# Performance work log

Measured on AMD Instinct MI355X. Metric: run time of the kernel, lower is better.

## Reference

```python
import jax, jax.numpy as jnp
import numpy as np

CLAMP_MIN = 1e-12
CLAMP_MAX = 1e12


def setup_inputs() -> dict:
    key = jax.random.key(0)
    k1, k2, k3 = jax.random.split(key, 3)
    N, C, H, W = 32, 11, 384, 384
    x = jax.random.normal(k1, (N, C, H, W), dtype=jnp.float32)
    centers = jax.random.normal(k2, (N, C, H, W), dtype=jnp.float32)
    labels = jax.random.randint(k3, (N, H, W), 0, C, dtype=jnp.int64)
    return {"x": x, "centers": centers, "labels": labels}


def reference(x, centers, labels):
    # x, centers: (N, C, H, W); labels: (N, H, W) int
    N, C, H, W = x.shape
    # res[n,c] = x[n,c]^2 + centers[n,c]^2 - 2 * x[n,c] @ centers[n,c]
    # (single batched matmul replaces the original per-(i,j) addmm loop)
    res = x * x + centers * centers - 2.0 * jnp.matmul(x, centers)
    # softmax over class dim, then max over class dim -> (N, H, W)
    res_max = jnp.max(jax.nn.softmax(res, axis=1), axis=1)
    dist = res_max * labels.astype(res_max.dtype)
    loss = jnp.sum(jnp.clip(dist, CLAMP_MIN, CLAMP_MAX)) / (H * W * N)
    return loss
```

## Files before the change

kernel.cpp:

```cpp
#include <hip/hip_runtime.h>
#include <stdint.h>

typedef __attribute__((ext_vector_type(8))) short short8;
typedef __attribute__((ext_vector_type(4))) float floatx4;
typedef __attribute__((ext_vector_type(4))) unsigned short u16x4;

#define Hh 384
#define Ww 384
#define Cc 11
#define Nn 32
#define PITCH 72

__device__ __forceinline__ unsigned short f2bf(float f) {
  union { float f; uint32_t u; } z; z.f = f;
  return (unsigned short)(z.u >> 16);
}
__device__ __forceinline__ float bf2f(unsigned short b) {
  union { uint32_t u; float f; } z; z.u = ((uint32_t)b) << 16;
  return z.f;
}

__global__ __launch_bounds__(256, 4)
void center_loss(const float* __restrict__ X, const float* __restrict__ Cen,
                 const int* __restrict__ Lab, float* __restrict__ Out) {
  __shared__ __align__(16) unsigned short Alds[64 * PITCH];
  __shared__ __align__(16) unsigned short Blds[64 * PITCH];
  __shared__ float red[4];

  const int bx   = blockIdx.x;
  const int xcd  = bx & 7;
  const int slot = bx >> 3;
  const int grp  = slot / 36;
  const int t36  = slot - grp * 36;
  const int n    = xcd + (grp << 3);
  const int ib = t36 / 6;
  const int jb = t36 - ib * 6;
  const int i0 = ib << 6, j0 = jb << 6;

  const int t   = threadIdx.x;
  const int l   = t & 63;
  const int w   = t >> 6;
  const int wr  = (w >> 1) << 5;
  const int wc  = (w & 1) << 5;
  const int q4  = l >> 4;
  const int l16 = l & 15;
  const int sa  = t & 15;
  const int sr  = t >> 4;

  const size_t plane = (size_t)Hh * Ww;
  const float* xbase = X   + (size_t)n * Cc * plane;
  const float* cbase = Cen + (size_t)n * Cc * plane;

  float m[16], s[16];
#pragma unroll
  for (int i = 0; i < 16; ++i) { m[i] = -3.0e38f; s[i] = 0.0f; }

  floatx4 acc[2][2];
  float ev[16];
#pragma unroll
  for (int a = 0; a < 2; ++a)
#pragma unroll
    for (int b = 0; b < 2; ++b) acc[a][b] = (floatx4){0.f, 0.f, 0.f, 0.f};
#pragma unroll
  for (int i = 0; i < 16; ++i) ev[i] = 0.0f;

  float4 pa[4];
  float  pb[16];

  {
    const float* ap = xbase + (size_t)(i0 + sr) * Ww + (sa << 2);
#pragma unroll
    for (int p = 0; p < 4; ++p)
      pa[p] = *reinterpret_cast<const float4*>(ap + (size_t)(p * 16) * Ww);
#pragma unroll
    for (int p = 0; p < 2; ++p) {
      const int kbase = (w << 3) + (p << 5);
      const float* bp = cbase + (size_t)kbase * Ww + j0 + l;
#pragma unroll
      for (int u = 0; u < 8; ++u) pb[p * 8 + u] = bp[(size_t)u * Ww];
    }
  }

  int c = 0, kb = 0;
  for (int it = 0; it < 66; ++it) {
    __syncthreads();

#pragma unroll
    for (int p = 0; p < 4; ++p) {
      u16x4 pk;
      pk.x = f2bf(pa[p].x); pk.y = f2bf(pa[p].y);
      pk.z = f2bf(pa[p].z); pk.w = f2bf(pa[p].w);
      *reinterpret_cast<u16x4*>(&Alds[(sr + 16 * p) * PITCH + (sa << 2)]) = pk;
    }
#pragma unroll
    for (int p = 0; p < 2; ++p) {
      const int kbase = (w << 3) + (p << 5);
      short8 pk;
#pragma unroll
      for (int u = 0; u < 8; ++u) pk[u] = (short)f2bf(pb[p * 8 + u]);
      *reinterpret_cast<short8*>(&Blds[l * PITCH + kbase]) = pk;
    }

    int kn = kb + 1, cn = c;
    if (kn == 6) { kn = 0; cn = c + 1; }
    float4 na[4];
    float  nb[16];
    if (it < 65) {
      const float* xb = xbase + (size_t)cn * plane;
      const float* cb = cbase + (size_t)cn * plane;
      const float* ap = xb + (size_t)(i0 + sr) * Ww + (kn << 6) + (sa << 2);
#pragma unroll
      for (int p = 0; p < 4; ++p)
        na[p] = *reinterpret_cast<const float4*>(ap + (size_t)(p * 16) * Ww);
#pragma unroll
      for (int p = 0; p < 2; ++p) {
        const int kbase = (w << 3) + (p << 5);
        const float* bp = cb + (size_t)((kn << 6) + kbase) * Ww + j0 + l;
#pragma unroll
        for (int u = 0; u < 8; ++u) nb[p * 8 + u] = bp[(size_t)u * Ww];
      }
    }

    __syncthreads();

    if (kb == jb) {
#pragma unroll
      for (int fr = 0; fr < 2; ++fr)
#pragma unroll
        for (int fc = 0; fc < 2; ++fc)
#pragma unroll
          for (int r = 0; r < 4; ++r) {
            const int idx = ((fr << 1) + fc) * 4 + r;
            const int pr = wr + (fr << 4) + (q4 << 2) + r;
            const int pc = wc + (fc << 4) + l16;
            float xv = bf2f(Alds[pr * PITCH + pc]);
            ev[idx] += xv * xv;
          }
    }
    if (kb == ib) {
#pragma unroll
      for (int fr = 0; fr < 2; ++fr)
#pragma unroll
        for (int fc = 0; fc < 2; ++fc)
#pragma unroll
          for (int r = 0; r < 4; ++r) {
            const int idx = ((fr << 1) + fc) * 4 + r;
            const int pr = wr + (fr << 4) + (q4 << 2) + r;
            const int pc = wc + (fc << 4) + l16;
            float cv = bf2f(Blds[pc * PITCH + pr]);
            ev[idx] += cv * cv;
          }
    }

#pragma unroll
    for (int ks = 0; ks < 2; ++ks) {
      const int ko = (ks << 5) + (q4 << 3);
      short8 a0 = *reinterpret_cast<const short8*>(&Alds[(wr +      l16) * PITCH + ko]);
      short8 a1 = *reinterpret_cast<const short8*>(&Alds[(wr + 16 + l16) * PITCH + ko]);
      short8 b0 = *reinterpret_cast<const short8*>(&Blds[(wc +      l16) * PITCH + ko]);
      short8 b1 = *reinterpret_cast<const short8*>(&Blds[(wc + 16 + l16) * PITCH + ko]);
      acc[0][0] = __builtin_amdgcn_mfma_f32_16x16x32_bf16(a0, b0, acc[0][0], 0, 0, 0);
      acc[0][1] = __builtin_amdgcn_mfma_f32_16x16x32_bf16(a0, b1, acc[0][1], 0, 0, 0);
      acc[1][0] = __builtin_amdgcn_mfma_f32_16x16x32_bf16(a1, b0, acc[1][0], 0, 0, 0);
      acc[1][1] = __builtin_amdgcn_mfma_f32_16x16x32_bf16(a1, b1, acc[1][1], 0, 0, 0);
    }

    if (kb == 5) {
#pragma unroll
      for (int fr = 0; fr < 2; ++fr)
#pragma unroll
        for (int fc = 0; fc < 2; ++fc)
#pragma unroll
          for (int r = 0; r < 4; ++r) {
            const int idx = ((fr << 1) + fc) * 4 + r;
            float res = ev[idx] - 2.0f * acc[fr][fc][r];
            float mi = m[idx];
            if (res <= mi) {
              s[idx] += __expf(res - mi);
            } else {
              s[idx] = s[idx] * __expf(mi - res) + 1.0f;
              m[idx] = res;
            }
            acc[fr][fc][r] = 0.0f;
            ev[idx] = 0.0f;
          }
    }

    kb = kn; c = cn;
#pragma unroll
    for (int p = 0; p < 4; ++p) pa[p] = na[p];
#pragma unroll
    for (int p = 0; p < 16; ++p) pb[p] = nb[p];
  }

  float local = 0.0f;
  const int* lb = Lab + (size_t)n * plane;
#pragma unroll
  for (int fr = 0; fr < 2; ++fr)
#pragma unroll
    for (int fc = 0; fc < 2; ++fc)
#pragma unroll
      for (int r = 0; r < 4; ++r) {
        const int idx = ((fr << 1) + fc) * 4 + r;
        const int pr = i0 + wr + (fr << 4) + (q4 << 2) + r;
        const int pc = j0 + wc + (fc << 4) + l16;
        float val = 1.0f / s[idx];
        float d = val * (float)lb[pr * Ww + pc];
        d = fminf(fmaxf(d, 1e-12f), 1e12f);
        local += d;
      }
#pragma unroll
  for (int off = 32; off > 0; off >>= 1) local += __shfl_down(local, off, 64);
  if (l == 0) red[w] = local;
  __syncthreads();
  if (t == 0) {
    float bs = (red[0] + red[1] + red[2] + red[3]) * (1.0f / 4718592.0f);
    atomicAdd(Out, bs);
  }
}

extern "C" void kernel_launch(void* const* d_in, const int* in_sizes, int n_in,
                              void* d_out, int out_size, void* d_ws, size_t ws_size,
                              hipStream_t stream) {
  const float* X   = (const float*)d_in[0];
  const float* Cen = (const float*)d_in[1];
  const int*   Lab = (const int*)d_in[2];
  float* Out = (float*)d_out;
  hipMemsetAsync(Out, 0, (size_t)out_size * sizeof(float), stream);
  hipLaunchKernelGGL(center_loss, dim3(Nn * 36), dim3(256), 0, stream,
                     X, Cen, Lab, Out);
}
```

Measured before the change: 495.7 us.

## Double-buffer LDS tiles with single barrier and fold norms into accumulator

Switches the A/B staging tiles to two LDS buffers so staging of the next tile overlaps compute of the current one, needing one custom barrier per tile that waits only on LDS counters. The squared-norm terms are subtracted directly into the MFMA accumulators instead of kept in separate registers. C-tile global loads become float2 per thread with a new thread mapping. LDS usage doubles, which may limit how many blocks fit per CU.

```diff
diff --git a/kernel.cpp b/kernel.cpp
--- a/kernel.cpp
+++ b/kernel.cpp
@@ -20,11 +20,17 @@
   return z.f;
 }
 
+#define BAR() do {                                          \
+    asm volatile("s_waitcnt lgkmcnt(0)" ::: "memory");      \
+    __builtin_amdgcn_s_barrier();                           \
+    asm volatile("" ::: "memory");                          \
+  } while (0)
+
 __global__ __launch_bounds__(256, 4)
 void center_loss(const float* __restrict__ X, const float* __restrict__ Cen,
                  const int* __restrict__ Lab, float* __restrict__ Out) {
-  __shared__ __align__(16) unsigned short Alds[64 * PITCH];
-  __shared__ __align__(16) unsigned short Blds[64 * PITCH];
+  __shared__ __align__(16) unsigned short Alds[2][64 * PITCH];
+  __shared__ __align__(16) unsigned short Blds[2][64 * PITCH];
   __shared__ float red[4];
 
   const int bx   = blockIdx.x;
@@ -44,154 +50,133 @@
   const int wc  = (w & 1) << 5;
   const int q4  = l >> 4;
   const int l16 = l & 15;
+  const int sr  = t >> 4;
   const int sa  = t & 15;
-  const int sr  = t >> 4;
+  const int jp  = t & 31;
+  const int kc  = t >> 5;
 
   const size_t plane = (size_t)Hh * Ww;
-  const float* xbase = X   + (size_t)n * Cc * plane;
-  const float* cbase = Cen + (size_t)n * Cc * plane;
+  const float* xrow = X   + (size_t)n * Cc * plane + (size_t)(i0 + sr) * Ww + (sa << 2);
+  const float* crow = Cen + (size_t)n * Cc * plane + (size_t)(kc << 3) * Ww + j0 + (jp << 1);
 
   float m[16], s[16];
 #pragma unroll
   for (int i = 0; i < 16; ++i) { m[i] = -3.0e38f; s[i] = 0.0f; }
 
   floatx4 acc[2][2];
-  float ev[16];
 #pragma unroll
   for (int a = 0; a < 2; ++a)
 #pragma unroll
     for (int b = 0; b < 2; ++b) acc[a][b] = (floatx4){0.f, 0.f, 0.f, 0.f};
-#pragma unroll
-  for (int i = 0; i < 16; ++i) ev[i] = 0.0f;
 
   float4 pa[4];
-  float  pb[16];
-
-  {
-    const float* ap = xbase + (size_t)(i0 + sr) * Ww + (sa << 2);
-#pragma unroll
-    for (int p = 0; p < 4; ++p)
-      pa[p] = *reinterpret_cast<const float4*>(ap + (size_t)(p * 16) * Ww);
-#pragma unroll
-    for (int p = 0; p < 2; ++p) {
-      const int kbase = (w << 3) + (p << 5);
-      const float* bp = cbase + (size_t)kbase * Ww + j0 + l;
-#pragma unroll
-      for (int u = 0; u < 8; ++u) pb[p * 8 + u] = bp[(size_t)u * Ww];
-    }
+  float2 pb[8];
+
+#define LOADT(CC, KK) do {                                                     \
+    const float* ap_ = xrow + (size_t)(CC) * plane + ((KK) << 6);              \
+    pa[0] = *reinterpret_cast<const float4*>(ap_);                             \
+    pa[1] = *reinterpret_cast<const float4*>(ap_ + 16 * Ww);                   \
+    pa[2] = *reinterpret_cast<const float4*>(ap_ + 32 * Ww);                   \
+    pa[3] = *reinterpret_cast<const float4*>(ap_ + 48 * Ww);                   \
+    const float* bp_ = crow + (size_t)(CC) * plane + (size_t)((KK) << 6) * Ww; \
+    _Pragma("unroll")                                                          \
+    for (int u_ = 0; u_ < 8; ++u_)                                             \
+      pb[u_] = *reinterpret_cast<const float2*>(bp_ + (size_t)u_ * Ww);        \
+  } while (0)
+
+#define STAGE(WB) do {                                                         \
+    _Pragma("unroll")                                                          \
+    for (int p_ = 0; p_ < 4; ++p_) {                                           \
+      u16x4 pk_;                                                               \
+      pk_.x = f2bf(pa[p_].x); pk_.y = f2bf(pa[p_].y);                          \
+      pk_.z = f2bf(pa[p_].z); pk_.w = f2bf(pa[p_].w);                          \
+      *reinterpret_cast<u16x4*>(&Alds[WB][(sr + 16 * p_) * PITCH + (sa << 2)]) = pk_; \
+    }                                                                          \
+    short8 s0_, s1_;                                                           \
+    _Pragma("unroll")                                                          \
+    for (int u_ = 0; u_ < 8; ++u_) {                                           \
+      s0_[u_] = (short)f2bf(pb[u_].x);                                         \
+      s1_[u_] = (short)f2bf(pb[u_].y);                                         \
+    }                                                                          \
+    *reinterpret_cast<short8*>(&Blds[WB][(jp << 1) * PITCH + (kc << 3)]) = s0_;       \
+    *reinterpret_cast<short8*>(&Blds[WB][((jp << 1) + 1) * PITCH + (kc << 3)]) = s1_; \
+  } while (0)
+
+#define COMPUTE(RB) do {                                                       \
+    if (kb == jb) {                       \
+      _Pragma("unroll") for (int fr_ = 0; fr_ < 2; ++fr_)                      \
+      _Pragma("unroll") for (int fc_ = 0; fc_ < 2; ++fc_)                      \
+      _Pragma("unroll") for (int r_ = 0; r_ < 4; ++r_) {                       \
+        const int pr_ = wr + (fr_ << 4) + (q4 << 2) + r_;                      \
+        const int pc_ = wc + (fc_ << 4) + l16;                                 \
+        float xv_ = bf2f(Alds[RB][pr_ * PITCH + pc_]);                         \
+        acc[fr_][fc_][r_] -= 0.5f * xv_ * xv_;                                 \
+      }                                                                        \
+    }                                                                          \
+    if (kb == ib) {         \
+      _Pragma("unroll") for (int fr_ = 0; fr_ < 2; ++fr_)                      \
+      _Pragma("unroll") for (int fc_ = 0; fc_ < 2; ++fc_)                      \
+      _Pragma("unroll") for (int r_ = 0; r_ < 4; ++r_) {                       \
+        const int pr_ = wr + (fr_ << 4) + (q4 << 2) + r_;                      \
+        const int pc_ = wc + (fc_ << 4) + l16;                                 \
+        float cv_ = bf2f(Blds[RB][pc_ * PITCH + pr_]);                         \
+        acc[fr_][fc_][r_] -= 0.5f * cv_ * cv_;                                 \
+      }                                                                        \
+    }                                                                          \
+    _Pragma("unroll") for (int ks_ = 0; ks_ < 2; ++ks_) {                      \
+      const int ko_ = (ks_ << 5) + (q4 << 3);                                  \
+      short8 a0_ = *reinterpret_cast<const short8*>(&Alds[RB][(wr +      l16) * PITCH + ko_]); \
+      short8 a1_ = *reinterpret_cast<const short8*>(&Alds[RB][(wr + 16 + l16) * PITCH + ko_]); \
+      short8 b0_ = *reinterpret_cast<const short8*>(&Blds[RB][(wc +      l16) * PITCH + ko_]); \
+      short8 b1_ = *reinterpret_cast<const short8*>(&Blds[RB][(wc + 16 + l16) * PITCH + ko_]); \
+      acc[0][0] = __builtin_amdgcn_mfma_f32_16x16x32_bf16(a0_, b0_, acc[0][0], 0, 0, 0); \
+      acc[0][1] = __builtin_amdgcn_mfma_f32_16x16x32_bf16(a0_, b1_, acc[0][1], 0, 0, 0); \
+      acc[1][0] = __builtin_amdgcn_mfma_f32_16x16x32_bf16(a1_, b0_, acc[1][0], 0, 0, 0); \
+      acc[1][1] = __builtin_amdgcn_mfma_f32_16x16x32_bf16(a1_, b1_, acc[1][1], 0, 0, 0); \
+    }                                                                          \
+    if (kb == 5) {                \
+      _Pragma("unroll") for (int fr_ = 0; fr_ < 2; ++fr_)                      \
+      _Pragma("unroll") for (int fc_ = 0; fc_ < 2; ++fc_)                      \
+      _Pragma("unroll") for (int r_ = 0; r_ < 4; ++r_) {                       \
+        const int idx_ = ((fr_ << 1) + fc_) * 4 + r_;                          \
+        float res_ = -2.0f * acc[fr_][fc_][r_];                                \
+        float mi_ = m[idx_];                                                   \
+        if (res_ <= mi_) {                                                     \
+          s[idx_] += __expf(res_ - mi_);                                       \
+        } else {                                                               \
+          s[idx_] = s[idx_] * __expf(mi_ - res_) + 1.0f;                       \
+          m[idx_] = res_;                                                      \
+        }                                                                      \
+        acc[fr_][fc_][r_] = 0.0f;                                              \
+      }                                                                        \
+    }                                                                          \
+    ++kb; if (kb == 6) kb = 0;                                                 \
+  } while (0)
+
+  LOADT(0, 0);
+  STAGE(0);
+  LOADT(0, 1);
+  BAR();
+
+  int kb = 0;
+  int kbL = 2, cL = 0;
+
+  for (int mi = 0; mi < 32; ++mi) {
+    STAGE(1);
+    LOADT(cL, kbL);
+    ++kbL; if (kbL == 6) { kbL = 0; ++cL; }
+    COMPUTE(0);
+    BAR();
+    STAGE(0);
+    LOADT(cL, kbL);
+    ++kbL; if (kbL == 6) { kbL = 0; ++cL; }
+    COMPUTE(1);
+    BAR();
   }
-
-  int c = 0, kb = 0;
-  for (int it = 0; it < 66; ++it) {
-    __syncthreads();
-
-#pragma unroll
-    for (int p = 0; p < 4; ++p) {
-      u16x4 pk;
-      pk.x = f2bf(pa[p].x); pk.y = f2bf(pa[p].y);
-      pk.z = f2bf(pa[p].z); pk.w = f2bf(pa[p].w);
-      *reinterpret_cast<u16x4*>(&Alds[(sr + 16 * p) * PITCH + (sa << 2)]) = pk;
-    }
-#pragma unroll
-    for (int p = 0; p < 2; ++p) {
-      const int kbase = (w << 3) + (p << 5);
-      short8 pk;
-#pragma unroll
-      for (int u = 0; u < 8; ++u) pk[u] = (short)f2bf(pb[p * 8 + u]);
-      *reinterpret_cast<short8*>(&Blds[l * PITCH + kbase]) = pk;
-    }
-
-    int kn = kb + 1, cn = c;
-    if (kn == 6) { kn = 0; cn = c + 1; }
-    float4 na[4];
-    float  nb[16];
-    if (it < 65) {
-      const float* xb = xbase + (size_t)cn * plane;
-      const float* cb = cbase + (size_t)cn * plane;
-      const float* ap = xb + (size_t)(i0 + sr) * Ww + (kn << 6) + (sa << 2);
-#pragma unroll
-      for (int p = 0; p < 4; ++p)
-        na[p] = *reinterpret_cast<const float4*>(ap + (size_t)(p * 16) * Ww);
-#pragma unroll
-      for (int p = 0; p < 2; ++p) {
-        const int kbase = (w << 3) + (p << 5);
-        const float* bp = cb + (size_t)((kn << 6) + kbase) * Ww + j0 + l;
-#pragma unroll
-        for (int u = 0; u < 8; ++u) nb[p * 8 + u] = bp[(size_t)u * Ww];
-      }
-    }
-
-    __syncthreads();
-
-    if (kb == jb) {
-#pragma unroll
-      for (int fr = 0; fr < 2; ++fr)
-#pragma unroll
-        for (int fc = 0; fc < 2; ++fc)
-#pragma unroll
-          for (int r = 0; r < 4; ++r) {
-            const int idx = ((fr << 1) + fc) * 4 + r;
-            const int pr = wr + (fr << 4) + (q4 << 2) + r;
-            const int pc = wc + (fc << 4) + l16;
-            float xv = bf2f(Alds[pr * PITCH + pc]);
-            ev[idx] += xv * xv;
-          }
-    }
-    if (kb == ib) {
-#pragma unroll
-      for (int fr = 0; fr < 2; ++fr)
-#pragma unroll
-        for (int fc = 0; fc < 2; ++fc)
-#pragma unroll
-          for (int r = 0; r < 4; ++r) {
-            const int idx = ((fr << 1) + fc) * 4 + r;
-            const int pr = wr + (fr << 4) + (q4 << 2) + r;
-            const int pc = wc + (fc << 4) + l16;
-            float cv = bf2f(Blds[pc * PITCH + pr]);
-            ev[idx] += cv * cv;
-          }
-    }
-
-#pragma unroll
-    for (int ks = 0; ks < 2; ++ks) {
-      const int ko = (ks << 5) + (q4 << 3);
-      short8 a0 = *reinterpret_cast<const short8*>(&Alds[(wr +      l16) * PITCH + ko]);
-      short8 a1 = *reinterpret_cast<const short8*>(&Alds[(wr + 16 + l16) * PITCH + ko]);
-      short8 b0 = *reinterpret_cast<const short8*>(&Blds[(wc +      l16) * PITCH + ko]);
-      short8 b1 = *reinterpret_cast<const short8*>(&Blds[(wc + 16 + l16) * PITCH + ko]);
-      acc[0][0] = __builtin_amdgcn_mfma_f32_16x16x32_bf16(a0, b0, acc[0][0], 0, 0, 0);
-      acc[0][1] = __builtin_amdgcn_mfma_f32_16x16x32_bf16(a0, b1, acc[0][1], 0, 0, 0);
-      acc[1][0] = __builtin_amdgcn_mfma_f32_16x16x32_bf16(a1, b0, acc[1][0], 0, 0, 0);
-      acc[1][1] = __builtin_amdgcn_mfma_f32_16x16x32_bf16(a1, b1, acc[1][1], 0, 0, 0);
-    }
-
-    if (kb == 5) {
-#pragma unroll
-      for (int fr = 0; fr < 2; ++fr)
-#pragma unroll
-        for (int fc = 0; fc < 2; ++fc)
-#pragma unroll
-          for (int r = 0; r < 4; ++r) {
-            const int idx = ((fr << 1) + fc) * 4 + r;
-            float res = ev[idx] - 2.0f * acc[fr][fc][r];
-            float mi = m[idx];
-            if (res <= mi) {
-              s[idx] += __expf(res - mi);
-            } else {
-              s[idx] = s[idx] * __expf(mi - res) + 1.0f;
-              m[idx] = res;
-            }
-            acc[fr][fc][r] = 0.0f;
-            ev[idx] = 0.0f;
-          }
-    }
-
-    kb = kn; c = cn;
-#pragma unroll
-    for (int p = 0; p < 4; ++p) pa[p] = na[p];
-#pragma unroll
-    for (int p = 0; p < 16; ++p) pb[p] = nb[p];
-  }
+  STAGE(1);
+  COMPUTE(0);
+  BAR();
+  COMPUTE(1);
 
   float local = 0.0f;
   const int* lb = Lab + (size_t)n * plane;
```

After: 506.6 us. 2.2% more time.

## Split class loop across two blocks with online-softmax partial merge

Applied to the files above, without the earlier changes.

Each (batch, tile) is split into two blocks that cover classes 0-5 and 6-10. Each block writes its running softmax max and sum per pixel to workspace, and a second merge kernel combines the two partials and applies the label reduction. This doubles the grid from 1152 blocks to improve occupancy and load balance across CUs. In exchange it adds workspace traffic (about 75MB of float2 partials written and read) and a second launch. The original single kernel is kept as a fallback when the workspace is too small.

```diff
diff --git a/kernel.cpp b/kernel.cpp
--- a/kernel.cpp
+++ b/kernel.cpp
@@ -21,15 +21,19 @@
 }
 
 __global__ __launch_bounds__(256, 4)
-void center_loss(const float* __restrict__ X, const float* __restrict__ Cen,
-                 const int* __restrict__ Lab, float* __restrict__ Out) {
+void center_partial(const float* __restrict__ X, const float* __restrict__ Cen,
+                    float2* __restrict__ Ws) {
   __shared__ __align__(16) unsigned short Alds[64 * PITCH];
   __shared__ __align__(16) unsigned short Blds[64 * PITCH];
-  __shared__ float red[4];
-
-  const int bx   = blockIdx.x;
-  const int xcd  = bx & 7;
-  const int slot = bx >> 3;
+
+  const int bx    = blockIdx.x;
+  const int chunk = (bx >= 1152) ? 1 : 0;
+  const int bxl   = bx - chunk * 1152;
+  const int c0    = chunk * 6;
+  const int NT    = chunk ? 30 : 36;
+
+  const int xcd  = bxl & 7;
+  const int slot = bxl >> 3;
   const int grp  = slot / 36;
   const int t36  = slot - grp * 36;
   const int n    = xcd + (grp << 3);
@@ -48,8 +52,8 @@
   const int sr  = t >> 4;
 
   const size_t plane = (size_t)Hh * Ww;
-  const float* xbase = X   + (size_t)n * Cc * plane;
-  const float* cbase = Cen + (size_t)n * Cc * plane;
+  const float* xbase = X   + ((size_t)n * Cc + c0) * plane;
+  const float* cbase = Cen + ((size_t)n * Cc + c0) * plane;
 
   float m[16], s[16];
 #pragma unroll
@@ -82,7 +86,7 @@
   }
 
   int c = 0, kb = 0;
-  for (int it = 0; it < 66; ++it) {
+  for (int it = 0; it < NT; ++it) {
     __syncthreads();
 
 #pragma unroll
@@ -105,7 +109,7 @@
     if (kn == 6) { kn = 0; cn = c + 1; }
     float4 na[4];
     float  nb[16];
-    if (it < 65) {
+    if (it < NT - 1) {
       const float* xb = xbase + (size_t)cn * plane;
       const float* cb = cbase + (size_t)cn * plane;
       const float* ap = xb + (size_t)(i0 + sr) * Ww + (kn << 6) + (sa << 2);
@@ -193,6 +197,212 @@
     for (int p = 0; p < 16; ++p) pb[p] = nb[p];
   }
 
+  float2* wsk = Ws + ((size_t)chunk * Nn + n) * plane;
+#pragma unroll
+  for (int fr = 0; fr < 2; ++fr)
+#pragma unroll
+    for (int fc = 0; fc < 2; ++fc)
+#pragma unroll
+      for (int r = 0; r < 4; ++r) {
+        const int idx = ((fr << 1) + fc) * 4 + r;
+        const int pr = i0 + wr + (fr << 4) + (q4 << 2) + r;
+        const int pc = j0 + wc + (fc << 4) + l16;
+        float2 v; v.x = m[idx]; v.y = s[idx];
+        wsk[(size_t)pr * Ww + pc] = v;
+      }
+}
+
+__global__ __launch_bounds__(256)
+void center_merge(const float2* __restrict__ Ws, const int* __restrict__ Lab,
+                  float* __restrict__ Out) {
+  __shared__ float red[4];
+  const size_t NP = (size_t)Nn * Hh * Ww;
+  const size_t stride = 4608ull * 256;
+  size_t e = (size_t)blockIdx.x * 256 + threadIdx.x;
+  float local = 0.0f;
+#pragma unroll
+  for (int u = 0; u < 4; ++u, e += stride) {
+    float2 a = Ws[e];
+    float2 b = Ws[NP + e];
+    float M = fmaxf(a.x, b.x);
+    float S = a.y * __expf(a.x - M) + b.y * __expf(b.x - M);
+    float d = (1.0f / S) * (float)Lab[e];
+    d = fminf(fmaxf(d, 1e-12f), 1e12f);
+    local += d;
+  }
+  const int l = threadIdx.x & 63, w = threadIdx.x >> 6;
+#pragma unroll
+  for (int off = 32; off > 0; off >>= 1) local += __shfl_down(local, off, 64);
+  if (l == 0) red[w] = local;
+  __syncthreads();
+  if (threadIdx.x == 0)
+    atomicAdd(Out, (red[0] + red[1] + red[2] + red[3]) * (1.0f / 4718592.0f));
+}
+
+__global__ __launch_bounds__(256, 4)
+void center_loss_mono(const float* __restrict__ X, const float* __restrict__ Cen,
+                      const int* __restrict__ Lab, float* __restrict__ Out) {
+  __shared__ __align__(16) unsigned short Alds[64 * PITCH];
+  __shared__ __align__(16) unsigned short Blds[64 * PITCH];
+  __shared__ float red[4];
+
+  const int bx   = blockIdx.x;
+  const int xcd  = bx & 7;
+  const int slot = bx >> 3;
+  const int grp  = slot / 36;
+  const int t36  = slot - grp * 36;
+  const int n    = xcd + (grp << 3);
+  const int ib = t36 / 6;
+  const int jb = t36 - ib * 6;
+  const int i0 = ib << 6, j0 = jb << 6;
+
+  const int t   = threadIdx.x;
+  const int l   = t & 63;
+  const int w   = t >> 6;
+  const int wr  = (w >> 1) << 5;
+  const int wc  = (w & 1) << 5;
+  const int q4  = l >> 4;
+  const int l16 = l & 15;
+  const int sa  = t & 15;
+  const int sr  = t >> 4;
+
+  const size_t plane = (size_t)Hh * Ww;
+  const float* xbase = X   + (size_t)n * Cc * plane;
+  const float* cbase = Cen + (size_t)n * Cc * plane;
+
+  float m[16], s[16];
+#pragma unroll
+  for (int i = 0; i < 16; ++i) { m[i] = -3.0e38f; s[i] = 0.0f; }
+  floatx4 acc[2][2];
+  float ev[16];
+#pragma unroll
+  for (int a = 0; a < 2; ++a)
+#pragma unroll
+    for (int b = 0; b < 2; ++b) acc[a][b] = (floatx4){0.f, 0.f, 0.f, 0.f};
+#pragma unroll
+  for (int i = 0; i < 16; ++i) ev[i] = 0.0f;
+
+  float4 pa[4];
+  float  pb[16];
+  {
+    const float* ap = xbase + (size_t)(i0 + sr) * Ww + (sa << 2);
+#pragma unroll
+    for (int p = 0; p < 4; ++p)
+      pa[p] = *reinterpret_cast<const float4*>(ap + (size_t)(p * 16) * Ww);
+#pragma unroll
+    for (int p = 0; p < 2; ++p) {
+      const int kbase = (w << 3) + (p << 5);
+      const float* bp = cbase + (size_t)kbase * Ww + j0 + l;
+#pragma unroll
+      for (int u = 0; u < 8; ++u) pb[p * 8 + u] = bp[(size_t)u * Ww];
+    }
+  }
+
+  int c = 0, kb = 0;
+  for (int it = 0; it < 66; ++it) {
+    __syncthreads();
+#pragma unroll
+    for (int p = 0; p < 4; ++p) {
+      u16x4 pk;
+      pk.x = f2bf(pa[p].x); pk.y = f2bf(pa[p].y);
+      pk.z = f2bf(pa[p].z); pk.w = f2bf(pa[p].w);
+      *reinterpret_cast<u16x4*>(&Alds[(sr + 16 * p) * PITCH + (sa << 2)]) = pk;
+    }
+#pragma unroll
+    for (int p = 0; p < 2; ++p) {
+      const int kbase = (w << 3) + (p << 5);
+      short8 pk;
+#pragma unroll
+      for (int u = 0; u < 8; ++u) pk[u] = (short)f2bf(pb[p * 8 + u]);
+      *reinterpret_cast<short8*>(&Blds[l * PITCH + kbase]) = pk;
+    }
+    int kn = kb + 1, cn = c;
+    if (kn == 6) { kn = 0; cn = c + 1; }
+    float4 na[4];
+    float  nb[16];
+    if (it < 65) {
+      const float* xb = xbase + (size_t)cn * plane;
+      const float* cb = cbase + (size_t)cn * plane;
+      const float* ap = xb + (size_t)(i0 + sr) * Ww + (kn << 6) + (sa << 2);
+#pragma unroll
+      for (int p = 0; p < 4; ++p)
+        na[p] = *reinterpret_cast<const float4*>(ap + (size_t)(p * 16) * Ww);
+#pragma unroll
+      for (int p = 0; p < 2; ++p) {
+        const int kbase = (w << 3) + (p << 5);
+        const float* bp = cb + (size_t)((kn << 6) + kbase) * Ww + j0 + l;
+#pragma unroll
+        for (int u = 0; u < 8; ++u) nb[p * 8 + u] = bp[(size_t)u * Ww];
+      }
+    }
+    __syncthreads();
+    if (kb == jb) {
+#pragma unroll
+      for (int fr = 0; fr < 2; ++fr)
+#pragma unroll
+        for (int fc = 0; fc < 2; ++fc)
+#pragma unroll
+          for (int r = 0; r < 4; ++r) {
+            const int idx = ((fr << 1) + fc) * 4 + r;
+            const int pr = wr + (fr << 4) + (q4 << 2) + r;
+            const int pc = wc + (fc << 4) + l16;
+            float xv = bf2f(Alds[pr * PITCH + pc]);
+            ev[idx] += xv * xv;
+          }
+    }
+    if (kb == ib) {
+#pragma unroll
+      for (int fr = 0; fr < 2; ++fr)
+#pragma unroll
+        for (int fc = 0; fc < 2; ++fc)
+#pragma unroll
+          for (int r = 0; r < 4; ++r) {
+            const int idx = ((fr << 1) + fc) * 4 + r;
+            const int pr = wr + (fr << 4) + (q4 << 2) + r;
+            const int pc = wc + (fc << 4) + l16;
+            float cv = bf2f(Blds[pc * PITCH + pr]);
+            ev[idx] += cv * cv;
+          }
+    }
+#pragma unroll
+    for (int ks = 0; ks < 2; ++ks) {
+      const int ko = (ks << 5) + (q4 << 3);
+      short8 a0 = *reinterpret_cast<const short8*>(&Alds[(wr +      l16) * PITCH + ko]);
+      short8 a1 = *reinterpret_cast<const short8*>(&Alds[(wr + 16 + l16) * PITCH + ko]);
+      short8 b0 = *reinterpret_cast<const short8*>(&Blds[(wc +      l16) * PITCH + ko]);
+      short8 b1 = *reinterpret_cast<const short8*>(&Blds[(wc + 16 + l16) * PITCH + ko]);
+      acc[0][0] = __builtin_amdgcn_mfma_f32_16x16x32_bf16(a0, b0, acc[0][0], 0, 0, 0);
+      acc[0][1] = __builtin_amdgcn_mfma_f32_16x16x32_bf16(a0, b1, acc[0][1], 0, 0, 0);
+      acc[1][0] = __builtin_amdgcn_mfma_f32_16x16x32_bf16(a1, b0, acc[1][0], 0, 0, 0);
+      acc[1][1] = __builtin_amdgcn_mfma_f32_16x16x32_bf16(a1, b1, acc[1][1], 0, 0, 0);
+    }
+    if (kb == 5) {
+#pragma unroll
+      for (int fr = 0; fr < 2; ++fr)
+#pragma unroll
+        for (int fc = 0; fc < 2; ++fc)
+#pragma unroll
+          for (int r = 0; r < 4; ++r) {
+            const int idx = ((fr << 1) + fc) * 4 + r;
+            float res = ev[idx] - 2.0f * acc[fr][fc][r];
+            float mi = m[idx];
+            if (res <= mi) {
+              s[idx] += __expf(res - mi);
+            } else {
+              s[idx] = s[idx] * __expf(mi - res) + 1.0f;
+              m[idx] = res;
+            }
+            acc[fr][fc][r] = 0.0f;
+            ev[idx] = 0.0f;
+          }
+    }
+    kb = kn; c = cn;
+#pragma unroll
+    for (int p = 0; p < 4; ++p) pa[p] = na[p];
+#pragma unroll
+    for (int p = 0; p < 16; ++p) pb[p] = nb[p];
+  }
+
   float local = 0.0f;
   const int* lb = Lab + (size_t)n * plane;
 #pragma unroll
@@ -227,6 +437,16 @@
   const int*   Lab = (const int*)d_in[2];
   float* Out = (float*)d_out;
   hipMemsetAsync(Out, 0, (size_t)out_size * sizeof(float), stream);
-  hipLaunchKernelGGL(center_loss, dim3(Nn * 36), dim3(256), 0, stream,
-                     X, Cen, Lab, Out);
-}
+
+  const size_t need = 2ull * Nn * Hh * Ww * sizeof(float2);
+  if (ws_size >= need && d_ws != nullptr) {
+    float2* Ws = (float2*)d_ws;
+    hipLaunchKernelGGL(center_partial, dim3(2 * Nn * 36), dim3(256), 0, stream,
+                       X, Cen, Ws);
+    hipLaunchKernelGGL(center_merge, dim3(4608), dim3(256), 0, stream,
+                       Ws, Lab, Out);
+  } else {
+    hipLaunchKernelGGL(center_loss_mono, dim3(Nn * 36), dim3(256), 0, stream,
+                       X, Cen, Lab, Out);
+  }
+}
```

After: 545.0 us. 1.1x slower.
